# Performance work log

Hardware: AMD Instinct MI355X
Metric: run time of the kernel (lower is better)

## Reference

```python
import jax, jax.numpy as jnp
import numpy as np

DIM = 256
MEM = 2048
N = 65536

def setup_inputs() -> dict:
    key = jax.random.key(0)
    ks = jax.random.split(key, 8)
    features = jax.random.normal(ks[0], (N, DIM), dtype=jnp.float32)
    coords = jax.random.uniform(ks[1], (N, 2), dtype=jnp.float32)
    memory = jax.random.normal(ks[2], (MEM, DIM), dtype=jnp.float32)
    # pos_mlp: Linear(2, dim) -> ReLU -> Linear(dim, dim); torch Linear: y = x @ W.T + b
    w1 = jax.random.normal(ks[3], (DIM, 2), dtype=jnp.float32) / jnp.sqrt(2.0)
    b1 = jax.random.normal(ks[4], (DIM,), dtype=jnp.float32) * 0.01
    w2 = jax.random.normal(ks[5], (DIM, DIM), dtype=jnp.float32) / jnp.sqrt(DIM * 1.0)
    b2 = jax.random.normal(ks[6], (DIM,), dtype=jnp.float32) * 0.01
    return {"features": features, "coords": coords, "memory": memory,
            "w1": w1, "b1": b1, "w2": w2, "b2": b2}

def reference(features, coords, memory, w1, b1, w2, b2):
    # tiny pos MLP on the mean coordinate -> [1, dim]
    mean_xy = jnp.mean(coords, axis=0, keepdims=True)            # [1, 2]
    h = jax.nn.relu(mean_xy @ w1.T + b1)                         # [1, dim]
    spatial_emb = h @ w2.T + b2                                  # [1, dim]
    z = features + spatial_emb                                   # [N, dim]
    scale = 1.0 / jnp.sqrt(jnp.asarray(features.shape[-1], features.dtype))
    scores = (z @ memory.T) * scale                              # [N, mem]
    attn = jax.nn.softmax(scores, axis=-1)
    return attn @ memory                                         # [N, dim]
```

## Files before the change

kernel.cpp:

```cpp
#include <hip/hip_runtime.h>
#include <hip/hip_bf16.h>

#define DIM 256
#define MEMN 2048
#define NROWS 65536
#define KVB 32
#define NT 64
#define TILE_B 32768

typedef __bf16 bf16x8 __attribute__((ext_vector_type(8)));
typedef float f32x4 __attribute__((ext_vector_type(4)));
typedef float f32x16 __attribute__((ext_vector_type(16)));
typedef unsigned int uint32x4 __attribute__((ext_vector_type(4)));

__global__ void prep_coords_kernel(const float* __restrict__ coords,
                                   float* __restrict__ partial) {
    __shared__ float red[512];
    int b = blockIdx.x, t = threadIdx.x;
    const f32x4* src = reinterpret_cast<const f32x4*>(coords + (size_t)b * 2048);
    f32x4 v0 = src[t * 2];
    f32x4 v1 = src[t * 2 + 1];
    red[t]       = v0[0] + v0[2] + v1[0] + v1[2];
    red[256 + t] = v0[1] + v0[3] + v1[1] + v1[3];
    __syncthreads();
    for (int s = 128; s > 0; s >>= 1) {
        if (t < s) { red[t] += red[t + s]; red[256 + t] += red[256 + t + s]; }
        __syncthreads();
    }
    if (t == 0) { partial[b] = red[0]; partial[64 + b] = red[256]; }
}

__global__ void prep_emb_kernel(const float* __restrict__ partial,
                                const float* __restrict__ w1,
                                const float* __restrict__ b1,
                                const float* __restrict__ w2,
                                const float* __restrict__ b2,
                                float* __restrict__ emb) {
    __shared__ float red[128];
    __shared__ float h[DIM];
    int t = threadIdx.x;
    if (t < 128) red[t] = partial[t];
    __syncthreads();
    for (int s = 32; s > 0; s >>= 1) {
        if (t < s) { red[t] += red[t + s]; red[64 + t] += red[64 + t + s]; }
        __syncthreads();
    }
    float mx = red[0] * (1.0f / NROWS);
    float my = red[64] * (1.0f / NROWS);
    float hv = mx * w1[2 * t] + my * w1[2 * t + 1] + b1[t];
    h[t] = hv > 0.f ? hv : 0.f;
    __syncthreads();
    float acc = b2[t];
    const float* wr = w2 + (size_t)t * DIM;
    #pragma unroll 4
    for (int k = 0; k < DIM; k += 4) {
        f32x4 wv = *reinterpret_cast<const f32x4*>(wr + k);
        acc += h[k] * wv[0] + h[k + 1] * wv[1] + h[k + 2] * wv[2] + h[k + 3] * wv[3];
    }
    emb[t] = acc;
}

__global__ void prep_blob_kernel(const float* __restrict__ mem,
                                 __bf16* __restrict__ blob) {
    __shared__ __bf16 ltile[KVB][DIM];
    int tile = blockIdx.x, t = threadIdx.x;
    int kt = tile * KVB;
    for (int c = t; c < 1024; c += 256) {
        int e = c * 8, row = e >> 8, col = e & 255;
        const float* s = mem + (size_t)(kt + row) * DIM + col;
        f32x4 a = *reinterpret_cast<const f32x4*>(s);
        f32x4 b = *reinterpret_cast<const f32x4*>(s + 4);
        bf16x8 o;
        #pragma unroll
        for (int j = 0; j < 4; ++j) { o[j] = (__bf16)a[j]; o[j + 4] = (__bf16)b[j]; }
        *reinterpret_cast<bf16x8*>(&ltile[row][col]) = o;
    }
    __syncthreads();
    __bf16* kb = blob + (size_t)tile * 16384;
    __bf16* vb = kb + 8192;
    for (int c = t; c < 1024; c += 256) {
        int e = c * 8, kv = e >> 8, x0 = e & 255;
        bf16x8 o = *reinterpret_cast<const bf16x8*>(&ltile[kv][x0 ^ (kv << 3)]);
        *reinterpret_cast<bf16x8*>(kb + e) = o;
    }
    for (int c = t; c < 1024; c += 256) {
        int idx = c * 8, R = idx >> 7, j0 = idx & 127;
        int L0 = j0 ^ ((R & 15) << 3);
        int d  = 4 * R + (L0 >> 5);
        int hh = (L0 >> 3) & 1;
        int ks = (L0 >> 4) & 1;
        int kvb = 4 * hh + 16 * ks;
        bf16x8 o;
        #pragma unroll
        for (int j = 0; j < 8; ++j) o[j] = ltile[kvb + (j & 3) + 8 * (j >> 2)][d];
        *reinterpret_cast<bf16x8*>(vb + idx) = o;
    }
}

__device__ __forceinline__ void gload_lds16(const void* g, void* l) {
    __builtin_amdgcn_global_load_lds(
        (const __attribute__((address_space(1))) unsigned int*)g,
        (__attribute__((address_space(3))) unsigned int*)l,
        16, 0, 0);
}

__device__ __forceinline__ unsigned int pkbf(float a, float b) {
    union { __bf16 h; unsigned short u; } ua, ub;
    ua.h = (__bf16)a; ub.h = (__bf16)b;
    return (unsigned int)ua.u | ((unsigned int)ub.u << 16);
}

__device__ __forceinline__ float fexp2(float x) {
#if __has_builtin(__builtin_amdgcn_exp2f)
    return __builtin_amdgcn_exp2f(x);
#else
    return exp2f(x);
#endif
}

__global__ __launch_bounds__(256, 2)
void flash_kernel(const float* __restrict__ feat,
                  const float* __restrict__ emb,
                  const __bf16* __restrict__ blob,
                  float* __restrict__ out) {
    __shared__ char smem[2 * TILE_B];

    const int t = threadIdx.x;
    const int w = t >> 6;
    const int lane = t & 63;
    const int ln = lane & 31;
    const int hi = lane >> 5;

    const int qrow = blockIdx.x * 128 + w * 32 + ln;

    const float QS = 0.0901684463f;
    bf16x8 qf[16];
    {
        const float* frow = feat + (size_t)qrow * DIM;
        #pragma unroll
        for (int kd = 0; kd < 16; ++kd) {
            int d0 = kd * 16 + hi * 8;
            f32x4 a = *reinterpret_cast<const f32x4*>(frow + d0);
            f32x4 b = *reinterpret_cast<const f32x4*>(frow + d0 + 4);
            f32x4 ea = *reinterpret_cast<const f32x4*>(emb + d0);
            f32x4 eb = *reinterpret_cast<const f32x4*>(emb + d0 + 4);
            bf16x8 q;
            #pragma unroll
            for (int i = 0; i < 4; ++i) {
                q[i]     = (__bf16)((a[i] + ea[i]) * QS);
                q[i + 4] = (__bf16)((b[i] + eb[i]) * QS);
            }
            qf[kd] = q;
        }
    }

    f32x16 o[8];
    #pragma unroll
    for (int dt = 0; dt < 8; ++dt) o[dt] = (f32x16)(0.f);
    float l = 0.f;

    const char* gsl = (const char*)blob + w * 8192 + lane * 16;
    char* bA = smem;
    char* bB = smem + TILE_B;

    f32x16 sa, sb;
    bf16x8 pb0, pb1;
    bf16x8 vpre[4];

    #define STAGE(k, buf)                                            \
        {   const char* _g = gsl + (size_t)(k) * TILE_B;             \
            char* _d = (buf) + w * 8192;                             \
            _Pragma("unroll")                                        \
            for (int _j = 0; _j < 8; ++_j)                           \
                gload_lds16(_g + _j * 1024, _d + _j * 1024);         \
        }

    #define KFRAG(buf, kd) \
        (*reinterpret_cast<const bf16x8*>((buf) + ln * 512 + ((((kd) * 16 + hi * 8) ^ (ln * 8)) << 1)))

    #define VFRAG(buf, dt, ks)                                                   \
        (*reinterpret_cast<const bf16x8*>((buf) + 16384 +                        \
            ((dt) * 8 + (ln >> 2)) * 256 +                                       \
            (((((ln & 3) * 32 + (ks) * 16 + hi * 8)) ^ ((((dt) * 8 + (ln >> 2)) & 15) << 3)) << 1)))

    #define SOFTMAX(PBUF)                                                        \
        {   f32x16 _s;                                                           \
            _Pragma("unroll")                                                    \
            for (int _e = 0; _e < 16; ++_e) _s[_e] = sa[_e] + sb[_e];            \
            float _la = 0.f;                                                     \
            _Pragma("unroll")                                                    \
            for (int _e = 0; _e < 16; ++_e) {                                    \
                float _p = fexp2(_s[_e]);                                        \
                _s[_e] = _p;                                                     \
                _la += _p;                                                       \
            }                                                                    \
            l += _la;                                                            \
            uint32x4 _f0, _f1;                                                   \
            _f0[0] = pkbf(_s[0], _s[1]);  _f0[1] = pkbf(_s[2], _s[3]);           \
            _f0[2] = pkbf(_s[4], _s[5]);  _f0[3] = pkbf(_s[6], _s[7]);           \
            _f1[0] = pkbf(_s[8], _s[9]);  _f1[1] = pkbf(_s[10], _s[11]);         \
            _f1[2] = pkbf(_s[12], _s[13]); _f1[3] = pkbf(_s[14], _s[15]);        \
            pb0 = __builtin_bit_cast(bf16x8, _f0);                               \
            pb1 = __builtin_bit_cast(bf16x8, _f1);                               \
            vpre[0] = VFRAG((PBUF), 0, 0);                                       \
            vpre[1] = VFRAG((PBUF), 0, 1);                                       \
            vpre[2] = VFRAG((PBUF), 1, 0);                                       \
            vpre[3] = VFRAG((PBUF), 1, 1);                                       \
        }

    STAGE(0, bA);
    asm volatile("s_waitcnt vmcnt(0)" ::: "memory");
    __builtin_amdgcn_s_barrier();
    asm volatile("" ::: "memory");
    sa = (f32x16)(-14.0f);
    sb = (f32x16)(0.f);
    __builtin_amdgcn_s_setprio(1);
    #pragma unroll
    for (int i = 0; i < 8; ++i) {
        sa = __builtin_amdgcn_mfma_f32_32x32x16_bf16(KFRAG(bA, 2 * i),     qf[2 * i],     sa, 0, 0, 0);
        sb = __builtin_amdgcn_mfma_f32_32x32x16_bf16(KFRAG(bA, 2 * i + 1), qf[2 * i + 1], sb, 0, 0, 0);
    }
    __builtin_amdgcn_s_setprio(0);
    STAGE(1, bB);
    SOFTMAX(bA);
    asm volatile("s_waitcnt vmcnt(0)" ::: "memory");
    __builtin_amdgcn_s_barrier();
    asm volatile("" ::: "memory");

    #pragma unroll 1
    for (int kt = 0; kt < NT - 1; ++kt) {
        sa = (f32x16)(-14.0f);
        sb = (f32x16)(0.f);
        __builtin_amdgcn_s_setprio(1);
        #pragma unroll
        for (int i = 0; i < 8; ++i) {
            sa = __builtin_amdgcn_mfma_f32_32x32x16_bf16(KFRAG(bB, 2 * i),     qf[2 * i],     sa, 0, 0, 0);
            o[i] = __builtin_amdgcn_mfma_f32_32x32x16_bf16(
                i < 2 ? vpre[2 * i] : VFRAG(bA, i, 0), pb0, o[i], 0, 0, 0);
            sb = __builtin_amdgcn_mfma_f32_32x32x16_bf16(KFRAG(bB, 2 * i + 1), qf[2 * i + 1], sb, 0, 0, 0);
            o[i] = __builtin_amdgcn_mfma_f32_32x32x16_bf16(
                i < 2 ? vpre[2 * i + 1] : VFRAG(bA, i, 1), pb1, o[i], 0, 0, 0);
        }
        __builtin_amdgcn_s_setprio(0);

        asm volatile("" ::: "memory");
        __builtin_amdgcn_s_barrier();
        asm volatile("" ::: "memory");

        if (kt + 2 < NT) STAGE(kt + 2, bA);
        SOFTMAX(bB);
        asm volatile("s_waitcnt vmcnt(0)" ::: "memory");
        __builtin_amdgcn_s_barrier();
        asm volatile("" ::: "memory");

        char* tmp = bA; bA = bB; bB = tmp;
    }

    __builtin_amdgcn_s_setprio(1);
    #pragma unroll
    for (int i = 0; i < 8; ++i) {
        o[i] = __builtin_amdgcn_mfma_f32_32x32x16_bf16(
            i < 2 ? vpre[2 * i] : VFRAG(bA, i, 0), pb0, o[i], 0, 0, 0);
        o[i] = __builtin_amdgcn_mfma_f32_32x32x16_bf16(
            i < 2 ? vpre[2 * i + 1] : VFRAG(bA, i, 1), pb1, o[i], 0, 0, 0);
    }
    __builtin_amdgcn_s_setprio(0);

    l += __shfl_xor(l, 32);
    float linv = 1.f / l;
    __syncthreads();
    #pragma unroll 1
    for (int ph = 0; ph < 2; ++ph) {
        if ((w >> 1) == ph) {
            char* base = smem + ((w & 1) * 32 + ln) * 1024;
            const int sw = (ln & 7) << 4;
            #pragma unroll
            for (int dt = 0; dt < 8; ++dt) {
                #pragma unroll
                for (int g = 0; g < 4; ++g) {
                    f32x4 v;
                    v[0] = o[dt][4 * g + 0] * linv;
                    v[1] = o[dt][4 * g + 1] * linv;
                    v[2] = o[dt][4 * g + 2] * linv;
                    v[3] = o[dt][4 * g + 3] * linv;
                    *reinterpret_cast<f32x4*>(base + ((dt * 128 + g * 32 + hi * 16) ^ sw)) = v;
                }
            }
        }
        __syncthreads();
        {
            char* gdst = (char*)out + ((size_t)blockIdx.x * 128 + ph * 64) * 1024;
            #pragma unroll
            for (int i = 0; i < 16; ++i) {
                int bo = t * 16 + i * 4096;
                int r = bo >> 10, off = bo & 1023;
                f32x4 v = *reinterpret_cast<const f32x4*>(
                    smem + r * 1024 + (off ^ ((r & 7) << 4)));
                *reinterpret_cast<f32x4*>(gdst + (size_t)r * 1024 + off) = v;
            }
        }
        __syncthreads();
    }
    #undef STAGE
    #undef KFRAG
    #undef VFRAG
    #undef SOFTMAX
}

extern "C" void kernel_launch(void* const* d_in, const int* in_sizes, int n_in,
                              void* d_out, int out_size, void* d_ws, size_t ws_size,
                              hipStream_t stream) {
    const float* features = (const float*)d_in[0];
    const float* coords   = (const float*)d_in[1];
    const float* memory   = (const float*)d_in[2];
    const float* w1       = (const float*)d_in[3];
    const float* b1       = (const float*)d_in[4];
    const float* w2       = (const float*)d_in[5];
    const float* b2       = (const float*)d_in[6];
    float* out = (float*)d_out;

    float*  partial = (float*)d_ws;
    float*  emb     = (float*)((char*)d_ws + 512);
    __bf16* blob    = (__bf16*)((char*)d_ws + 2048);

    prep_coords_kernel<<<64, 256, 0, stream>>>(coords, partial);
    prep_blob_kernel<<<NT, 256, 0, stream>>>(memory, blob);
    prep_emb_kernel<<<1, 256, 0, stream>>>(partial, w1, b1, w2, b2, emb);
    flash_kernel<<<NROWS / 128, 256, 0, stream>>>(features, emb, blob, out);
}
```

Before: 203.6 us.

## Split K/V staging into separate buffers with triple-buffered V and one barrier

Splits each 32 KB KV tile into separate K and V halves: K is double-buffered and V triple-buffered in 80 KB of LDS. The next tile's loads are issued at the top of the loop, and a partial vmcnt wait lets the two barriers per iteration become one. The V prefetch into registers is dropped. The aim is to hide global-to-LDS latency behind the MFMA work and cut synchronisation, at the cost of more LDS, which may limit occupancy to two blocks per CU.

```diff
diff --git a/kernel.cpp b/kernel.cpp
--- a/kernel.cpp
+++ b/kernel.cpp
@@ -7,6 +7,7 @@
 #define KVB 32
 #define NT 64
 #define TILE_B 32768
+#define PART_B 16384
 
 typedef __bf16 bf16x8 __attribute__((ext_vector_type(8)));
 typedef float f32x4 __attribute__((ext_vector_type(4)));
@@ -123,7 +124,7 @@
                   const float* __restrict__ emb,
                   const __bf16* __restrict__ blob,
                   float* __restrict__ out) {
-    __shared__ char smem[2 * TILE_B];
+    __shared__ char smem[5 * PART_B];
 
     const int t = threadIdx.x;
     const int w = t >> 6;
@@ -159,31 +160,41 @@
     for (int dt = 0; dt < 8; ++dt) o[dt] = (f32x16)(0.f);
     float l = 0.f;
 
-    const char* gsl = (const char*)blob + w * 8192 + lane * 16;
-    char* bA = smem;
-    char* bB = smem + TILE_B;
+    char* kA = smem;
+    char* kB = smem + PART_B;
+    char* vA = smem + 2 * PART_B;
+    char* vB = smem + 3 * PART_B;
+    char* vC = smem + 4 * PART_B;
 
     f32x16 sa, sb;
     bf16x8 pb0, pb1;
-    bf16x8 vpre[4];
-
-    #define STAGE(k, buf)                                            \
-        {   const char* _g = gsl + (size_t)(k) * TILE_B;             \
-            char* _d = (buf) + w * 8192;                             \
-            _Pragma("unroll")                                        \
-            for (int _j = 0; _j < 8; ++_j)                           \
-                gload_lds16(_g + _j * 1024, _d + _j * 1024);         \
+
+    #define STAGE_K(k, buf)                                                   \
+        {   const char* _g = (const char*)blob + (size_t)(k) * TILE_B         \
+                             + w * 4096 + lane * 16;                          \
+            char* _d = (buf) + w * 4096;                                      \
+            _Pragma("unroll")                                                 \
+            for (int _j = 0; _j < 4; ++_j)                                    \
+                gload_lds16(_g + _j * 1024, _d + _j * 1024);                  \
+        }
+    #define STAGE_V(k, buf)                                                   \
+        {   const char* _g = (const char*)blob + (size_t)(k) * TILE_B         \
+                             + PART_B + w * 4096 + lane * 16;                 \
+            char* _d = (buf) + w * 4096;                                      \
+            _Pragma("unroll")                                                 \
+            for (int _j = 0; _j < 4; ++_j)                                    \
+                gload_lds16(_g + _j * 1024, _d + _j * 1024);                  \
         }
 
     #define KFRAG(buf, kd) \
         (*reinterpret_cast<const bf16x8*>((buf) + ln * 512 + ((((kd) * 16 + hi * 8) ^ (ln * 8)) << 1)))
 
     #define VFRAG(buf, dt, ks)                                                   \
-        (*reinterpret_cast<const bf16x8*>((buf) + 16384 +                        \
+        (*reinterpret_cast<const bf16x8*>((buf) +                                \
             ((dt) * 8 + (ln >> 2)) * 256 +                                       \
             (((((ln & 3) * 32 + (ks) * 16 + hi * 8)) ^ ((((dt) * 8 + (ln >> 2)) & 15) << 3)) << 1)))
 
-    #define SOFTMAX(PBUF)                                                        \
+    #define SOFTMAX()                                                            \
         {   f32x16 _s;                                                           \
             _Pragma("unroll")                                                    \
             for (int _e = 0; _e < 16; ++_e) _s[_e] = sa[_e] + sb[_e];            \
@@ -202,13 +213,12 @@
             _f1[2] = pkbf(_s[12], _s[13]); _f1[3] = pkbf(_s[14], _s[15]);        \
             pb0 = __builtin_bit_cast(bf16x8, _f0);                               \
             pb1 = __builtin_bit_cast(bf16x8, _f1);                               \
-            vpre[0] = VFRAG((PBUF), 0, 0);                                       \
-            vpre[1] = VFRAG((PBUF), 0, 1);                                       \
-            vpre[2] = VFRAG((PBUF), 1, 0);                                       \
-            vpre[3] = VFRAG((PBUF), 1, 1);                                       \
-        }
-
-    STAGE(0, bA);
+        }
+
+    STAGE_K(0, kA);
+    STAGE_K(1, kB);
+    STAGE_V(0, vA);
+    STAGE_V(1, vB);
     asm volatile("s_waitcnt vmcnt(0)" ::: "memory");
     __builtin_amdgcn_s_barrier();
     asm volatile("" ::: "memory");
@@ -217,52 +227,53 @@
     __builtin_amdgcn_s_setprio(1);
     #pragma unroll
     for (int i = 0; i < 8; ++i) {
-        sa = __builtin_amdgcn_mfma_f32_32x32x16_bf16(KFRAG(bA, 2 * i),     qf[2 * i],     sa, 0, 0, 0);
-        sb = __builtin_amdgcn_mfma_f32_32x32x16_bf16(KFRAG(bA, 2 * i + 1), qf[2 * i + 1], sb, 0, 0, 0);
+        sa = __builtin_amdgcn_mfma_f32_32x32x16_bf16(KFRAG(kA, 2 * i),     qf[2 * i],     sa, 0, 0, 0);
+        sb = __builtin_amdgcn_mfma_f32_32x32x16_bf16(KFRAG(kA, 2 * i + 1), qf[2 * i + 1], sb, 0, 0, 0);
     }
     __builtin_amdgcn_s_setprio(0);
-    STAGE(1, bB);
-    SOFTMAX(bA);
-    asm volatile("s_waitcnt vmcnt(0)" ::: "memory");
+    SOFTMAX();
+    asm volatile("" ::: "memory");
     __builtin_amdgcn_s_barrier();
     asm volatile("" ::: "memory");
 
     #pragma unroll 1
     for (int kt = 0; kt < NT - 1; ++kt) {
+        if (kt + 2 < NT) {
+            STAGE_K(kt + 2, kA);
+            STAGE_V(kt + 2, vC);
+        }
+
         sa = (f32x16)(-14.0f);
         sb = (f32x16)(0.f);
         __builtin_amdgcn_s_setprio(1);
         #pragma unroll
         for (int i = 0; i < 8; ++i) {
-            sa = __builtin_amdgcn_mfma_f32_32x32x16_bf16(KFRAG(bB, 2 * i),     qf[2 * i],     sa, 0, 0, 0);
-            o[i] = __builtin_amdgcn_mfma_f32_32x32x16_bf16(
-                i < 2 ? vpre[2 * i] : VFRAG(bA, i, 0), pb0, o[i], 0, 0, 0);
-            sb = __builtin_amdgcn_mfma_f32_32x32x16_bf16(KFRAG(bB, 2 * i + 1), qf[2 * i + 1], sb, 0, 0, 0);
-            o[i] = __builtin_amdgcn_mfma_f32_32x32x16_bf16(
-                i < 2 ? vpre[2 * i + 1] : VFRAG(bA, i, 1), pb1, o[i], 0, 0, 0);
+            sa = __builtin_amdgcn_mfma_f32_32x32x16_bf16(KFRAG(kB, 2 * i),     qf[2 * i],     sa, 0, 0, 0);
+            o[i] = __builtin_amdgcn_mfma_f32_32x32x16_bf16(VFRAG(vA, i, 0), pb0, o[i], 0, 0, 0);
+            sb = __builtin_amdgcn_mfma_f32_32x32x16_bf16(KFRAG(kB, 2 * i + 1), qf[2 * i + 1], sb, 0, 0, 0);
+            o[i] = __builtin_amdgcn_mfma_f32_32x32x16_bf16(VFRAG(vA, i, 1), pb1, o[i], 0, 0, 0);
         }
         __builtin_amdgcn_s_setprio(0);
 
-        asm volatile("" ::: "memory");
+        SOFTMAX();
+
+        if (kt + 2 < NT) {
+            asm volatile("s_waitcnt vmcnt(4)" ::: "memory");
+        } else {
+            asm volatile("s_waitcnt vmcnt(0)" ::: "memory");
+        }
         __builtin_amdgcn_s_barrier();
         asm volatile("" ::: "memory");
 
-        if (kt + 2 < NT) STAGE(kt + 2, bA);
-        SOFTMAX(bB);
-        asm volatile("s_waitcnt vmcnt(0)" ::: "memory");
-        __builtin_amdgcn_s_barrier();
-        asm volatile("" ::: "memory");
-
-        char* tmp = bA; bA = bB; bB = tmp;
+        char* ktmp = kA; kA = kB; kB = ktmp;
+        char* vtmp = vA; vA = vB; vB = vC; vC = vtmp;
     }
 
     __builtin_amdgcn_s_setprio(1);
     #pragma unroll
     for (int i = 0; i < 8; ++i) {
-        o[i] = __builtin_amdgcn_mfma_f32_32x32x16_bf16(
-            i < 2 ? vpre[2 * i] : VFRAG(bA, i, 0), pb0, o[i], 0, 0, 0);
-        o[i] = __builtin_amdgcn_mfma_f32_32x32x16_bf16(
-            i < 2 ? vpre[2 * i + 1] : VFRAG(bA, i, 1), pb1, o[i], 0, 0, 0);
+        o[i] = __builtin_amdgcn_mfma_f32_32x32x16_bf16(VFRAG(vA, i, 0), pb0, o[i], 0, 0, 0);
+        o[i] = __builtin_amdgcn_mfma_f32_32x32x16_bf16(VFRAG(vA, i, 1), pb1, o[i], 0, 0, 0);
     }
     __builtin_amdgcn_s_setprio(0);
 
@@ -301,7 +312,8 @@
         }
         __syncthreads();
     }
-    #undef STAGE
+    #undef STAGE_K
+    #undef STAGE_V
     #undef KFRAG
     #undef VFRAG
     #undef SOFTMAX
```

After: 195.1 us. -4.2%, faster.
